# Performance work log

Hardware: AMD Instinct MI355X
Metric: run time of the kernel (lower is better)

The kernel has to match this reference:

```python
import jax, jax.numpy as jnp
import numpy as np

TOP_K = 8
SCORE_FUNC = "sigmoid"
ROUTE_NORM = True
ROUTE_SCALE = 2.5


def setup_inputs() -> dict:
    key = jax.random.key(0)
    k1, k2, k3 = jax.random.split(key, 3)
    B, S, H, E = 4, 4096, 2048, 64
    hidden_states = jax.random.normal(k1, (B, S, H), dtype=jnp.float32)
    # nn.Linear default init scale ~ 1/sqrt(H); exact distribution irrelevant for correctness
    gate_w = jax.random.normal(k2, (E, H), dtype=jnp.float32) * (1.0 / np.sqrt(H))
    expert_bias = jax.random.normal(k3, (E,), dtype=jnp.float32) * 0.1
    return {"hidden_states": hidden_states, "expert_bias": expert_bias, "gate_w": gate_w}


def reference(hidden_states, expert_bias, gate_w):
    B, S, H = hidden_states.shape
    x = hidden_states.reshape(-1, H)  # [T, H]
    logits = jnp.einsum("th,eh->te", x, gate_w)  # [T, E]
    if SCORE_FUNC == "sigmoid":
        scores = jax.nn.sigmoid(logits.astype(jnp.float32))
    else:
        scores = jax.nn.softmax(logits.astype(jnp.float32), axis=-1)
    if expert_bias is not None:
        _, selected_experts = jax.lax.top_k(scores + expert_bias[None, :], TOP_K)
        top_scores = jnp.take_along_axis(scores, selected_experts, axis=1)
    else:
        top_scores, selected_experts = jax.lax.top_k(scores, TOP_K)
    if SCORE_FUNC == "sigmoid" and ROUTE_NORM:
        denom = jnp.sum(top_scores, axis=-1, keepdims=True) + 1e-20
        top_scores = top_scores / denom
    top_scores = top_scores * ROUTE_SCALE
    return top_scores, selected_experts
```

## Files before the change

kernel.cpp:

```cpp
#include <hip/hip_runtime.h>
#include <math.h>

#define T_TOTAL 16384
#define HDIM    2048
#define NEXP    64

typedef unsigned short ushort_t;
using bf16x8 = __attribute__((ext_vector_type(8))) short;
using f32x4  = __attribute__((ext_vector_type(4))) float;

__device__ __forceinline__ unsigned cvtpk_bf16(float a, float b) {
    unsigned r;
    asm("v_cvt_pk_bf16_f32 %0, %1, %2" : "=v"(r) : "v"(a), "v"(b));
    return r;
}

__device__ __forceinline__ void split8(const float4 a, const float4 b,
                                       bf16x8& h, bf16x8& m, bf16x8& l) {
    const float f[8] = {a.x, a.y, a.z, a.w, b.x, b.y, b.z, b.w};
    union { unsigned u[4]; bf16x8 v; } H, M, L;
#pragma unroll
    for (int d = 0; d < 4; ++d) {
        const float f0 = f[2*d], f1 = f[2*d+1];
        const unsigned ph = cvtpk_bf16(f0, f1);
        const float r0 = f0 - __uint_as_float(ph << 16);
        const float r1 = f1 - __uint_as_float(ph & 0xFFFF0000u);
        const unsigned pm = cvtpk_bf16(r0, r1);
        const float s0 = r0 - __uint_as_float(pm << 16);
        const float s1 = r1 - __uint_as_float(pm & 0xFFFF0000u);
        H.u[d] = ph;
        M.u[d] = pm;
        L.u[d] = cvtpk_bf16(s0, s1);
    }
    h = H.v; m = M.v; l = L.v;
}

__device__ __forceinline__ void load_lds16(const float* g, float* lds) {
    __builtin_amdgcn_global_load_lds(
        (const __attribute__((address_space(1))) unsigned int*)g,
        (__attribute__((address_space(3))) unsigned int*)lds, 16, 0, 0);
}

__global__ __launch_bounds__(256, 2)
void router_fused(const float* __restrict__ x,
                  const float* __restrict__ w,
                  const float* __restrict__ bias,
                  float* __restrict__ out_scores,
                  float* __restrict__ out_idx)
{
    __shared__ __align__(16) float S[4 * 4096];

    const int tid  = threadIdx.x;
    const int wv   = tid >> 6;
    const int lane = tid & 63;
    const int t0   = blockIdx.x * 32;
    const int k0   = wv * 512;
    const int lr   = lane & 15;
    const int lg   = lane >> 4;

    float* Wbase = S + wv * 4096;

    const int wrow = lane >> 3;
    const int wchk = (lane & 7) ^ wrow;
    const float* wg = w + (size_t)wrow * HDIM + k0 + wchk * 4;

    const float* px0 = x + (size_t)(t0 + lr) * HDIM + k0 + lg * 8;
    const float* px1 = px0 + (size_t)16 * HDIM;

    f32x4 acc[2][4];
#pragma unroll
    for (int mt = 0; mt < 2; ++mt)
#pragma unroll
        for (int nt = 0; nt < 4; ++nt) {
            f32x4 z = {0.0f, 0.0f, 0.0f, 0.0f};
            acc[mt][nt] = z;
        }

#pragma unroll
    for (int p = 0; p < 8; ++p)
        load_lds16(wg + (size_t)(p * 8) * HDIM, Wbase + p * 256);

    float4 c00 = *(const float4*)(px0);
    float4 c01 = *(const float4*)(px0 + 4);
    float4 c10 = *(const float4*)(px1);
    float4 c11 = *(const float4*)(px1 + 4);

#pragma unroll 1
    for (int kk = 0; kk < 16; ++kk) {
        bf16x8 Ah[2], Am[2], Al[2];
        split8(c00, c01, Ah[0], Am[0], Al[0]);
        split8(c10, c11, Ah[1], Am[1], Al[1]);

        const int kn = ((kk + 1) & 15) * 32;

        c00 = *(const float4*)(px0 + kn);
        c01 = *(const float4*)(px0 + kn + 4);
        c10 = *(const float4*)(px1 + kn);
        c11 = *(const float4*)(px1 + kn + 4);

        float* wd = Wbase + ((kk + 1) & 1) * 2048;
#pragma unroll
        for (int p = 0; p < 8; ++p)
            load_lds16(wg + (size_t)(p * 8) * HDIM + kn, wd + p * 256);

        asm volatile("s_waitcnt vmcnt(12)" ::: "memory");

        const float* Wc = Wbase + (kk & 1) * 2048;
#pragma unroll
        for (int nt = 0; nt < 4; ++nt) {
            const int e  = nt * 16 + lr;
            const int sw = lr & 7;
            const float* rb = Wc + e * 32;
            const float4 b0 = *(const float4*)(rb + (((2 * lg)     ^ sw) * 4));
            const float4 b1 = *(const float4*)(rb + (((2 * lg + 1) ^ sw) * 4));
            bf16x8 Bh, Bm, Bl;
            split8(b0, b1, Bh, Bm, Bl);
#pragma unroll
            for (int mt = 0; mt < 2; ++mt) {
                acc[mt][nt] = __builtin_amdgcn_mfma_f32_16x16x32_bf16(Ah[mt], Bh, acc[mt][nt], 0, 0, 0);
                acc[mt][nt] = __builtin_amdgcn_mfma_f32_16x16x32_bf16(Am[mt], Bh, acc[mt][nt], 0, 0, 0);
                acc[mt][nt] = __builtin_amdgcn_mfma_f32_16x16x32_bf16(Al[mt], Bh, acc[mt][nt], 0, 0, 0);
                acc[mt][nt] = __builtin_amdgcn_mfma_f32_16x16x32_bf16(Ah[mt], Bm, acc[mt][nt], 0, 0, 0);
                acc[mt][nt] = __builtin_amdgcn_mfma_f32_16x16x32_bf16(Am[mt], Bm, acc[mt][nt], 0, 0, 0);
                acc[mt][nt] = __builtin_amdgcn_mfma_f32_16x16x32_bf16(Ah[mt], Bl, acc[mt][nt], 0, 0, 0);
            }
        }
    }

    const float bv = bias[lane];

    asm volatile("s_waitcnt vmcnt(0)" ::: "memory");

#pragma unroll
    for (int mt = 0; mt < 2; ++mt)
#pragma unroll
        for (int nt = 0; nt < 4; ++nt)
#pragma unroll
            for (int r = 0; r < 4; ++r)
                S[wv * 4096 + (mt * 16 + lg * 4 + r) * 64 + nt * 16 + lr] = acc[mt][nt][r];

    __syncthreads();

#pragma unroll 1
    for (int i = 0; i < 8; ++i) {
        const int t = wv * 8 + i;
        const int o = t * 64 + lane;
        const float logit = S[o] + S[4096 + o] + S[8192 + o] + S[12288 + o];

        const float score = 1.0f / (1.0f + expf(-logit));
        float key = score + bv;

        float myscore = 0.0f;
        int   myidx   = 0;
        float denom   = 0.0f;

#pragma unroll
        for (int r = 0; r < 8; ++r) {
            float bk = key;
#pragma unroll
            for (int off = 32; off > 0; off >>= 1)
                bk = fmaxf(bk, __shfl_xor(bk, off));
            const unsigned long long msk = __ballot(key == bk);
            const int bi = __ffsll((long long)msk) - 1;
            const float wsc = __shfl(score, bi);
            denom += wsc;
            if (lane == r)  { myscore = wsc; myidx = bi; }
            if (lane == bi) key = -__builtin_inff();
        }

        const float factor = 2.5f / (denom + 1e-20f);
        if (lane < 8) {
            out_scores[(size_t)(t0 + t) * 8 + lane] = myscore * factor;
            out_idx  [(size_t)(t0 + t) * 8 + lane] = (float)myidx;
        }
    }
}

extern "C" void kernel_launch(void* const* d_in, const int* in_sizes, int n_in,
                              void* d_out, int out_size, void* d_ws, size_t ws_size,
                              hipStream_t stream)
{
    const float* x    = (const float*)d_in[0];
    const float* bias = (const float*)d_in[1];
    const float* w    = (const float*)d_in[2];

    float* out = (float*)d_out;

    router_fused<<<dim3(T_TOTAL / 32), dim3(256), 0, stream>>>(
        x, w, bias, out, out + (size_t)T_TOTAL * 8);
}
```

Baseline: 217.0 us.

## Pre-split gate weights into bf16 triplets and restructure GEMM across waves

A small pre-kernel converts the fp32 gate weights once per call into swizzled bf16 hi/mid/lo planes in workspace, so the main kernel no longer re-splits W in every block. The main kernel now splits the output tile across waves by token and expert halves instead of splitting K, and stages both X and W through double-buffered LDS with block barriers. This removes the cross-wave K reduction. It adds two extra MFMA terms (Al*Bm, Am*Bl) for accuracy. A naive fallback path covers the case where the workspace is too small.

```diff
diff --git a/kernel.cpp b/kernel.cpp
--- a/kernel.cpp
+++ b/kernel.cpp
@@ -35,117 +35,150 @@
     h = H.v; m = M.v; l = L.v;
 }
 
-__device__ __forceinline__ void load_lds16(const float* g, float* lds) {
+__device__ __forceinline__ void load_lds16(const void* g, void* lds) {
     __builtin_amdgcn_global_load_lds(
         (const __attribute__((address_space(1))) unsigned int*)g,
         (__attribute__((address_space(3))) unsigned int*)lds, 16, 0, 0);
 }
 
+__device__ __forceinline__ int xswz(int row) {
+    return ((row & 7) << 1) | ((row >> 3) & 1);
+}
+
+__global__ __launch_bounds__(256)
+void convert_w_kernel(const float* __restrict__ w, ushort_t* __restrict__ wt)
+{
+    const int idx = blockIdx.x * 256 + threadIdx.x;
+    const int e   = idx >> 8;
+    const int c8  = idx & 255;
+    const int kc  = c8 >> 3;
+    const int c   = c8 & 7;
+
+    const float* src = w + (size_t)e * HDIM + kc * 64 + c * 8;
+    const float4 v0 = *(const float4*)(src);
+    const float4 v1 = *(const float4*)(src + 4);
+    bf16x8 H, M, L;
+    split8(v0, v1, H, M, L);
+
+    const int slot = c ^ (e & 7);
+    bf16x8* base = (bf16x8*)wt;
+    base[((size_t)(kc * 3 + 0) * 64 + e) * 8 + slot] = H;
+    base[((size_t)(kc * 3 + 1) * 64 + e) * 8 + slot] = M;
+    base[((size_t)(kc * 3 + 2) * 64 + e) * 8 + slot] = L;
+}
+
 __global__ __launch_bounds__(256, 2)
 void router_fused(const float* __restrict__ x,
-                  const float* __restrict__ w,
+                  const ushort_t* __restrict__ wt,
                   const float* __restrict__ bias,
                   float* __restrict__ out_scores,
                   float* __restrict__ out_idx)
 {
-    __shared__ __align__(16) float S[4 * 4096];
+    __shared__ __align__(16) float    Xs[2][32 * 64];
+    __shared__ __align__(16) ushort_t Ws[2][3 * 64 * 64];
 
     const int tid  = threadIdx.x;
     const int wv   = tid >> 6;
     const int lane = tid & 63;
     const int t0   = blockIdx.x * 32;
-    const int k0   = wv * 512;
+    const int a    = wv >> 1;
+    const int b    = wv & 1;
     const int lr   = lane & 15;
     const int lg   = lane >> 4;
 
-    float* Wbase = S + wv * 4096;
-
-    const int wrow = lane >> 3;
-    const int wchk = (lane & 7) ^ wrow;
-    const float* wg = w + (size_t)wrow * HDIM + k0 + wchk * 4;
-
-    const float* px0 = x + (size_t)(t0 + lr) * HDIM + k0 + lg * 8;
-    const float* px1 = px0 + (size_t)16 * HDIM;
-
-    f32x4 acc[2][4];
-#pragma unroll
-    for (int mt = 0; mt < 2; ++mt)
-#pragma unroll
-        for (int nt = 0; nt < 4; ++nt) {
-            f32x4 z = {0.0f, 0.0f, 0.0f, 0.0f};
-            acc[mt][nt] = z;
+    const float bv = bias[lane];
+
+    const int xrow0 = wv * 8 + (lane >> 4);
+    const int xrow1 = xrow0 + 4;
+    const float* xsrc0 = x + (size_t)(t0 + xrow0) * HDIM + ((lane & 15) ^ xswz(xrow0)) * 4;
+    const float* xsrc1 = x + (size_t)(t0 + xrow1) * HDIM + ((lane & 15) ^ xswz(xrow1)) * 4;
+
+    const ushort_t* wsrc = wt + (size_t)(wv * 6) * 512 + lane * 8;
+
+    f32x4 acc[8];
+#pragma unroll
+    for (int i = 0; i < 8; ++i) {
+        f32x4 z = {0.0f, 0.0f, 0.0f, 0.0f};
+        acc[i] = z;
+    }
+
+    const int rowX = a * 16 + lr;
+    const int swzX = xswz(rowX);
+
+    auto stage = [&](int kc, int bi) {
+        const int ko = kc * 64;
+        load_lds16(xsrc0 + ko, &Xs[bi][(wv * 2 + 0) * 256]);
+        load_lds16(xsrc1 + ko, &Xs[bi][(wv * 2 + 1) * 256]);
+        const ushort_t* wn = wsrc + (size_t)kc * 12288;
+#pragma unroll
+        for (int q = 0; q < 6; ++q)
+            load_lds16(wn + q * 512, &Ws[bi][(wv * 6 + q) * 512]);
+    };
+
+#define COMPUTE(BI, PAR) do {                                                 \
+    const float*  rb  = &Xs[BI][rowX * 64];                                   \
+    const bf16x8* wbp = (const bf16x8*)&Ws[BI][0];                            \
+    _Pragma("unroll")                                                         \
+    for (int ks = 0; ks < 2; ++ks) {                                          \
+        const int g0 = ks * 8 + lg * 2;                                       \
+        const float4 c0 = *(const float4*)(rb + ((g0       ^ swzX) * 4));     \
+        const float4 c1 = *(const float4*)(rb + (((g0 + 1) ^ swzX) * 4));     \
+        bf16x8 Ah, Am, Al;                                                    \
+        split8(c0, c1, Ah, Am, Al);                                           \
+        _Pragma("unroll")                                                     \
+        for (int n = 0; n < 2; ++n) {                                         \
+            const int e    = b * 32 + n * 16 + lr;                            \
+            const int slot = (ks * 4 + lg) ^ (e & 7);                         \
+            const bf16x8 Bh = wbp[(0 * 64 + e) * 8 + slot];                   \
+            const bf16x8 Bm = wbp[(1 * 64 + e) * 8 + slot];                   \
+            const bf16x8 Bl = wbp[(2 * 64 + e) * 8 + slot];                   \
+            f32x4 t = acc[(PAR) * 4 + ks * 2 + n];                            \
+            t = __builtin_amdgcn_mfma_f32_16x16x32_bf16(Ah, Bh, t, 0, 0, 0);  \
+            t = __builtin_amdgcn_mfma_f32_16x16x32_bf16(Am, Bh, t, 0, 0, 0);  \
+            t = __builtin_amdgcn_mfma_f32_16x16x32_bf16(Ah, Bm, t, 0, 0, 0);  \
+            t = __builtin_amdgcn_mfma_f32_16x16x32_bf16(Am, Bm, t, 0, 0, 0);  \
+            t = __builtin_amdgcn_mfma_f32_16x16x32_bf16(Al, Bh, t, 0, 0, 0);  \
+            t = __builtin_amdgcn_mfma_f32_16x16x32_bf16(Ah, Bl, t, 0, 0, 0);  \
+            t = __builtin_amdgcn_mfma_f32_16x16x32_bf16(Al, Bm, t, 0, 0, 0);  \
+            t = __builtin_amdgcn_mfma_f32_16x16x32_bf16(Am, Bl, t, 0, 0, 0);  \
+            acc[(PAR) * 4 + ks * 2 + n] = t;                                  \
+        }                                                                     \
+    }                                                                         \
+} while (0)
+
+    stage(0, 0);
+    __syncthreads();
+
+#pragma unroll 1
+    for (int j = 0; j < 16; ++j) {
+        const int kc0 = j * 2;
+        stage(kc0 + 1, 1);
+        COMPUTE(0, 0);
+        __syncthreads();
+        if (kc0 + 2 < 32) stage(kc0 + 2, 0);
+        COMPUTE(1, 1);
+        __syncthreads();
+    }
+#undef COMPUTE
+
+    float* ov = &Xs[0][0];
+#pragma unroll
+    for (int n = 0; n < 2; ++n) {
+        const f32x4 s = (acc[0 * 4 + 0 * 2 + n] + acc[0 * 4 + 1 * 2 + n])
+                      + (acc[1 * 4 + 0 * 2 + n] + acc[1 * 4 + 1 * 2 + n]);
+#pragma unroll
+        for (int r = 0; r < 4; ++r) {
+            const int t = a * 16 + lg * 4 + r;
+            const int e = b * 32 + n * 16 + lr;
+            ov[t * 64 + e] = s[r];
         }
-
-#pragma unroll
-    for (int p = 0; p < 8; ++p)
-        load_lds16(wg + (size_t)(p * 8) * HDIM, Wbase + p * 256);
-
-    float4 c00 = *(const float4*)(px0);
-    float4 c01 = *(const float4*)(px0 + 4);
-    float4 c10 = *(const float4*)(px1);
-    float4 c11 = *(const float4*)(px1 + 4);
-
-#pragma unroll 1
-    for (int kk = 0; kk < 16; ++kk) {
-        bf16x8 Ah[2], Am[2], Al[2];
-        split8(c00, c01, Ah[0], Am[0], Al[0]);
-        split8(c10, c11, Ah[1], Am[1], Al[1]);
-
-        const int kn = ((kk + 1) & 15) * 32;
-
-        c00 = *(const float4*)(px0 + kn);
-        c01 = *(const float4*)(px0 + kn + 4);
-        c10 = *(const float4*)(px1 + kn);
-        c11 = *(const float4*)(px1 + kn + 4);
-
-        float* wd = Wbase + ((kk + 1) & 1) * 2048;
-#pragma unroll
-        for (int p = 0; p < 8; ++p)
-            load_lds16(wg + (size_t)(p * 8) * HDIM + kn, wd + p * 256);
-
-        asm volatile("s_waitcnt vmcnt(12)" ::: "memory");
-
-        const float* Wc = Wbase + (kk & 1) * 2048;
-#pragma unroll
-        for (int nt = 0; nt < 4; ++nt) {
-            const int e  = nt * 16 + lr;
-            const int sw = lr & 7;
-            const float* rb = Wc + e * 32;
-            const float4 b0 = *(const float4*)(rb + (((2 * lg)     ^ sw) * 4));
-            const float4 b1 = *(const float4*)(rb + (((2 * lg + 1) ^ sw) * 4));
-            bf16x8 Bh, Bm, Bl;
-            split8(b0, b1, Bh, Bm, Bl);
-#pragma unroll
-            for (int mt = 0; mt < 2; ++mt) {
-                acc[mt][nt] = __builtin_amdgcn_mfma_f32_16x16x32_bf16(Ah[mt], Bh, acc[mt][nt], 0, 0, 0);
-                acc[mt][nt] = __builtin_amdgcn_mfma_f32_16x16x32_bf16(Am[mt], Bh, acc[mt][nt], 0, 0, 0);
-                acc[mt][nt] = __builtin_amdgcn_mfma_f32_16x16x32_bf16(Al[mt], Bh, acc[mt][nt], 0, 0, 0);
-                acc[mt][nt] = __builtin_amdgcn_mfma_f32_16x16x32_bf16(Ah[mt], Bm, acc[mt][nt], 0, 0, 0);
-                acc[mt][nt] = __builtin_amdgcn_mfma_f32_16x16x32_bf16(Am[mt], Bm, acc[mt][nt], 0, 0, 0);
-                acc[mt][nt] = __builtin_amdgcn_mfma_f32_16x16x32_bf16(Ah[mt], Bl, acc[mt][nt], 0, 0, 0);
-            }
-        }
-    }
-
-    const float bv = bias[lane];
-
-    asm volatile("s_waitcnt vmcnt(0)" ::: "memory");
-
-#pragma unroll
-    for (int mt = 0; mt < 2; ++mt)
-#pragma unroll
-        for (int nt = 0; nt < 4; ++nt)
-#pragma unroll
-            for (int r = 0; r < 4; ++r)
-                S[wv * 4096 + (mt * 16 + lg * 4 + r) * 64 + nt * 16 + lr] = acc[mt][nt][r];
-
+    }
     __syncthreads();
 
 #pragma unroll 1
     for (int i = 0; i < 8; ++i) {
         const int t = wv * 8 + i;
-        const int o = t * 64 + lane;
-        const float logit = S[o] + S[4096 + o] + S[8192 + o] + S[12288 + o];
+        const float logit = ov[t * 64 + lane];
 
         const float score = 1.0f / (1.0f + expf(-logit));
         float key = score + bv;
@@ -176,6 +209,51 @@
     }
 }
 
+__global__ void router_gemm_naive(const float* __restrict__ x,
+                                  const float* __restrict__ w,
+                                  float* __restrict__ partial)
+{
+    const int t = blockIdx.x;
+    const int e = threadIdx.x;
+    const float* xp = x + (size_t)t * HDIM;
+    const float* wp = w + (size_t)e * HDIM;
+    float s = 0.0f;
+    for (int k = 0; k < HDIM; ++k) s = fmaf(xp[k], wp[k], s);
+    partial[(size_t)t * NEXP + e] = s;
+}
+
+__global__ __launch_bounds__(256)
+void router_topk_naive(const float* __restrict__ partial,
+                       const float* __restrict__ bias,
+                       float* __restrict__ out_scores,
+                       float* __restrict__ out_idx)
+{
+    const int token = blockIdx.x * 4 + (threadIdx.x >> 6);
+    const int lane  = threadIdx.x & 63;
+    const float logit = partial[(size_t)token * NEXP + lane];
+    const float score = 1.0f / (1.0f + expf(-logit));
+    float key = score + bias[lane];
+    float myscore = 0.0f; int myidx = 0; float denom = 0.0f;
+#pragma unroll
+    for (int r = 0; r < 8; ++r) {
+        float bk = key;
+#pragma unroll
+        for (int off = 32; off > 0; off >>= 1)
+            bk = fmaxf(bk, __shfl_xor(bk, off));
+        const unsigned long long msk = __ballot(key == bk);
+        const int bi = __ffsll((long long)msk) - 1;
+        const float wsc = __shfl(score, bi);
+        denom += wsc;
+        if (lane == r)  { myscore = wsc; myidx = bi; }
+        if (lane == bi) key = -__builtin_inff();
+    }
+    const float factor = 2.5f / (denom + 1e-20f);
+    if (lane < 8) {
+        out_scores[(size_t)token * 8 + lane] = myscore * factor;
+        out_idx  [(size_t)token * 8 + lane] = (float)myidx;
+    }
+}
+
 extern "C" void kernel_launch(void* const* d_in, const int* in_sizes, int n_in,
                               void* d_out, int out_size, void* d_ws, size_t ws_size,
                               hipStream_t stream)
@@ -186,6 +264,17 @@
 
     float* out = (float*)d_out;
 
-    router_fused<<<dim3(T_TOTAL / 32), dim3(256), 0, stream>>>(
-        x, w, bias, out, out + (size_t)T_TOTAL * 8);
-}
+    const size_t wtBytes = (size_t)3 * NEXP * HDIM * sizeof(ushort_t);
+
+    if (ws_size >= wtBytes) {
+        ushort_t* wt = (ushort_t*)d_ws;
+        convert_w_kernel<<<dim3(64), dim3(256), 0, stream>>>(w, wt);
+        router_fused<<<dim3(T_TOTAL / 32), dim3(256), 0, stream>>>(
+            x, wt, bias, out, out + (size_t)T_TOTAL * 8);
+    } else {
+        float* partial = (float*)d_ws;
+        router_gemm_naive<<<dim3(T_TOTAL), dim3(64), 0, stream>>>(x, w, partial);
+        router_topk_naive<<<dim3(T_TOTAL / 4), dim3(256), 0, stream>>>(
+            partial, bias, out, out + (size_t)T_TOTAL * 8);
+    }
+}
```

Result: slower. 229.3 us (+5.7%).
